# Optimization experiments

Hardware: AMD Instinct MI355X
Metric: run time of the kernel (lower is better)

Reference implementation:

```python
import jax, jax.numpy as jnp
import numpy as np

N = 100000      # nodes
E = 1600000     # edges (avg degree 16)
DIN = 512
DOUT = 64
NEG_SLOPE = 0.2


def spmm(rows, cols, vals, x, n):
    # sparse [n,n] (COO) @ dense [n,d]: out[r] += vals[e] * x[cols[e]]
    return jax.ops.segment_sum(vals[:, None] * x[cols], rows, num_segments=n)


def setup_inputs() -> dict:
    key = jax.random.key(0)
    k1, k2, k3, k4, k5 = jax.random.split(key, 5)
    features = jax.random.normal(k1, (N, DIN), dtype=jnp.float32)
    edge_rows = jax.random.randint(k2, (E,), 0, N, dtype=jnp.int32)
    edge_cols = jax.random.randint(k3, (E,), 0, N, dtype=jnp.int32)
    edge_vals = jax.random.uniform(k4, (E,), dtype=jnp.float32)
    limit = float(np.sqrt(6.0 / (DIN + DOUT)))  # xavier_uniform
    weight = jax.random.uniform(k5, (DIN, DOUT), dtype=jnp.float32,
                                minval=-limit, maxval=limit)
    return {"features": features, "weight": weight,
            "edge_rows": edge_rows, "edge_cols": edge_cols,
            "edge_vals": edge_vals}


def reference(features, weight, edge_rows, edge_cols, edge_vals):
    # active=True path: fused dense mm + LeakyReLU(0.2)
    support = jax.nn.leaky_relu(features @ weight, negative_slope=NEG_SLOPE)
    output = spmm(edge_rows, edge_cols, edge_vals, support, N)  # adj @ support
    az = spmm(edge_rows, edge_cols, edge_vals, output, N)       # adj @ output
    return (output, az)
```

## Files before the change

kernel.cpp:

```cpp
#include <hip/hip_runtime.h>
#include <hip/hip_bf16.h>

#define DIN 512
#define DOUT 64

typedef float float4v __attribute__((ext_vector_type(4)));
typedef float f32x4 __attribute__((ext_vector_type(4)));
typedef _Float16 f16x8 __attribute__((ext_vector_type(8)));
typedef unsigned int uint4v __attribute__((ext_vector_type(4)));

static __device__ __forceinline__ unsigned int pk_f16(float a, float b) {
  return __builtin_bit_cast(unsigned int, __builtin_amdgcn_cvt_pkrtz(a, b));
}

__global__ __launch_bounds__(256) void gemm_mfma_kernel(
    const float* __restrict__ X, const float* __restrict__ W,
    float* __restrict__ sup, int N)
{
  __shared__ unsigned int wlds[128][68];

  const int t    = threadIdx.x;
  const int wv   = t >> 6;
  const int lane = t & 63;
  const int l15  = lane & 15;
  const int g    = lane >> 4;

  const int rb   = blockIdx.x * 64 + wv * 16;
  const int rA   = rb + l15;
  const int rowA = rA < N ? rA : N - 1;
  const float* __restrict__ xrow = X + (size_t)rowA * DIN;

  f32x4 acc[4];
#pragma unroll
  for (int f = 0; f < 4; ++f) acc[f] = (f32x4)0.0f;

#pragma unroll 1
  for (int kh = 0; kh < 2; ++kh) {
    const int kbase = kh * 256;
    __syncthreads();
#pragma unroll
    for (int i = 0; i < 32; ++i) {
      const int idx = t + i * 256;
      const int c = idx & 63;
      const int p = idx >> 6;
      const float w0 = W[(size_t)(kbase + 2 * p) * DOUT + c];
      const float w1 = W[(size_t)(kbase + 2 * p + 1) * DOUT + c];
      wlds[p][c] = pk_f16(w0, w1);
    }
    __syncthreads();

#pragma unroll
    for (int s = 0; s < 8; ++s) {
      const int k0 = kbase + s * 32;
      const f32x4 a0 = *reinterpret_cast<const f32x4*>(xrow + k0 + g * 8);
      const f32x4 a1 = *reinterpret_cast<const f32x4*>(xrow + k0 + g * 8 + 4);
      uint4v au;
      au[0] = pk_f16(a0[0], a0[1]);
      au[1] = pk_f16(a0[2], a0[3]);
      au[2] = pk_f16(a1[0], a1[1]);
      au[3] = pk_f16(a1[2], a1[3]);
      const f16x8 afrag = __builtin_bit_cast(f16x8, au);

      const int pb = s * 16 + g * 4;
#pragma unroll
      for (int f = 0; f < 4; ++f) {
        const int c = f * 16 + l15;
        uint4v bu;
        bu[0] = wlds[pb + 0][c];
        bu[1] = wlds[pb + 1][c];
        bu[2] = wlds[pb + 2][c];
        bu[3] = wlds[pb + 3][c];
        const f16x8 bfrag = __builtin_bit_cast(f16x8, bu);
        acc[f] = __builtin_amdgcn_mfma_f32_16x16x32_f16(afrag, bfrag, acc[f], 0, 0, 0);
      }
    }
  }

  const int r0 = rb + g * 4;
#pragma unroll
  for (int f = 0; f < 4; ++f) {
    const int c = f * 16 + l15;
#pragma unroll
    for (int reg = 0; reg < 4; ++reg) {
      const int r = r0 + reg;
      if (r < N) {
        const float v = acc[f][reg];
        sup[(size_t)r * DOUT + c] = v > 0.0f ? v : 0.2f * v;
      }
    }
  }
}

__global__ __launch_bounds__(256) void hist_kernel(
    const int* __restrict__ er, int* __restrict__ cnt, int E)
{
  int i = blockIdx.x * blockDim.x + threadIdx.x;
  const int stride = gridDim.x * blockDim.x;
  for (; i < E; i += stride) atomicAdd(&cnt[er[i]], 1);
}

__global__ __launch_bounds__(256) void scan_block_kernel(
    const int* __restrict__ in, int* __restrict__ out,
    int* __restrict__ bsum, int n)
{
  __shared__ int s[256];
  const int t = threadIdx.x;
  const int gid = blockIdx.x * 256 + t;
  const int v = gid < n ? in[gid] : 0;
  s[t] = v;
  __syncthreads();
#pragma unroll
  for (int off = 1; off < 256; off <<= 1) {
    const int add = t >= off ? s[t - off] : 0;
    __syncthreads();
    s[t] += add;
    __syncthreads();
  }
  if (gid < n) out[gid] = s[t] - v;
  if (t == 255) bsum[blockIdx.x] = s[255];
}

__global__ __launch_bounds__(256) void scan_bsums_kernel(int* __restrict__ bsum, int nb)
{
  __shared__ int s[256];
  __shared__ int carry_s;
  const int t = threadIdx.x;
  if (t == 0) carry_s = 0;
  __syncthreads();
  for (int base = 0; base < nb; base += 256) {
    const int i = base + t;
    const int v = i < nb ? bsum[i] : 0;
    s[t] = v;
    __syncthreads();
#pragma unroll
    for (int off = 1; off < 256; off <<= 1) {
      const int add = t >= off ? s[t - off] : 0;
      __syncthreads();
      s[t] += add;
      __syncthreads();
    }
    const int carry = carry_s;
    if (i < nb) bsum[i] = s[t] - v + carry;
    const int total = s[255];
    __syncthreads();
    if (t == 0) carry_s = carry + total;
    __syncthreads();
  }
}

__global__ __launch_bounds__(256) void scan_add_kernel(
    int* __restrict__ out, const int* __restrict__ bsum, int n)
{
  const int gid = blockIdx.x * 256 + threadIdx.x;
  if (gid < n) out[gid] += bsum[blockIdx.x];
}

__global__ __launch_bounds__(256) void scatter_kernel(
    const int* __restrict__ er, const int* __restrict__ ec,
    const float* __restrict__ ev, int* __restrict__ cursor,
    int* __restrict__ scols, float* __restrict__ svals, int E)
{
  int i = blockIdx.x * blockDim.x + threadIdx.x;
  const int stride = gridDim.x * blockDim.x;
  for (; i < E; i += stride) {
    const int r = er[i];
    const int pos = atomicAdd(&cursor[r], 1);
    scols[pos] = ec[i];
    svals[pos] = ev[i];
  }
}

__global__ __launch_bounds__(256) void spmm_csr_kernel(
    const int* __restrict__ rowptr, const int* __restrict__ scols,
    const float* __restrict__ svals, const float* __restrict__ x,
    float* __restrict__ out, int N)
{
  const int lane = threadIdx.x & 63;
  const int row  = blockIdx.x * 4 + (threadIdx.x >> 6);
  if (row >= N) return;

  const int s = rowptr[row];
  const int e = rowptr[row + 1];
  float acc = 0.0f;

  int i = s;
  for (; i + 4 <= e; i += 4) {
    const int b = __builtin_amdgcn_readfirstlane(i);
    const int c0 = scols[b],     c1 = scols[b + 1];
    const int c2 = scols[b + 2], c3 = scols[b + 3];
    const float v0 = svals[b],     v1 = svals[b + 1];
    const float v2 = svals[b + 2], v3 = svals[b + 3];
    const float x0 = x[(size_t)c0 * DOUT + lane];
    const float x1 = x[(size_t)c1 * DOUT + lane];
    const float x2 = x[(size_t)c2 * DOUT + lane];
    const float x3 = x[(size_t)c3 * DOUT + lane];
    acc = fmaf(v0, x0, acc);
    acc = fmaf(v1, x1, acc);
    acc = fmaf(v2, x2, acc);
    acc = fmaf(v3, x3, acc);
  }
  for (; i < e; ++i) {
    const int b = __builtin_amdgcn_readfirstlane(i);
    acc = fmaf(svals[b], x[(size_t)scols[b] * DOUT + lane], acc);
  }

  out[(size_t)row * DOUT + lane] = acc;
}

extern "C" void kernel_launch(void* const* d_in, const int* in_sizes, int n_in,
                              void* d_out, int out_size, void* d_ws, size_t ws_size,
                              hipStream_t stream)
{
  const float* X  = (const float*)d_in[0];
  const float* W  = (const float*)d_in[1];
  const int*   er = (const int*)d_in[2];
  const int*   ec = (const int*)d_in[3];
  const float* ev = (const float*)d_in[4];

  const int N = in_sizes[0] / DIN;
  const int E = in_sizes[2];
  const size_t half = (size_t)N * DOUT;

  char* w = (char*)d_ws;
  float* sup    = (float*)w;                 w += half * sizeof(float);
  int*   rowptr = (int*)w;                   w += (size_t)(N + 1) * sizeof(int);
  int*   cursor = (int*)w;                   w += (size_t)(N + 1) * sizeof(int);
  int*   bsum   = (int*)w;                   w += 1024 * sizeof(int);
  int*   scols  = (int*)w;                   w += (size_t)E * sizeof(int);
  float* svals  = (float*)w;

  float* out0 = (float*)d_out;
  float* out1 = out0 + half;

  const int n_scan = N + 1;
  const int nb = (n_scan + 255) / 256;

  (void)hipMemsetAsync(cursor, 0, (size_t)n_scan * sizeof(int), stream);
  hist_kernel<<<2048, 256, 0, stream>>>(er, cursor, E);
  scan_block_kernel<<<nb, 256, 0, stream>>>(cursor, rowptr, bsum, n_scan);
  scan_bsums_kernel<<<1, 256, 0, stream>>>(bsum, nb);
  scan_add_kernel<<<nb, 256, 0, stream>>>(rowptr, bsum, n_scan);
  (void)hipMemcpyAsync(cursor, rowptr, (size_t)n_scan * sizeof(int),
                       hipMemcpyDeviceToDevice, stream);
  scatter_kernel<<<2048, 256, 0, stream>>>(er, ec, ev, cursor, scols, svals, E);

  gemm_mfma_kernel<<<(N + 63) / 64, 256, 0, stream>>>(X, W, sup, N);

  spmm_csr_kernel<<<(N + 3) / 4, 256, 0, stream>>>(rowptr, scols, svals, sup, out0, N);
  spmm_csr_kernel<<<(N + 3) / 4, 256, 0, stream>>>(rowptr, scols, svals, out0, out1, N);
}
```

Measured before the change: 388.0 us.

## Prepack fp16 weights, prefetch A rows, vector LDS loads, unroll SpMM by 8

A new small kernel converts the weight matrix once into packed fp16 pairs in column-major order. The GEMM can then fill LDS with 128-bit copies and read B fragments with one vector LDS load instead of four scalar ones. The GEMM now issues all A-row loads for a K-half before the LDS barrier so global latency overlaps the weight staging, at the cost of more registers. The SpMM gains an 8-wide unrolled gather loop to keep more memory loads in flight, and the change adds one extra kernel launch.

```diff
diff --git a/kernel.cpp b/kernel.cpp
--- a/kernel.cpp
+++ b/kernel.cpp
@@ -4,7 +4,6 @@
 #define DIN 512
 #define DOUT 64
 
-typedef float float4v __attribute__((ext_vector_type(4)));
 typedef float f32x4 __attribute__((ext_vector_type(4)));
 typedef _Float16 f16x8 __attribute__((ext_vector_type(8)));
 typedef unsigned int uint4v __attribute__((ext_vector_type(4)));
@@ -13,11 +12,21 @@
   return __builtin_bit_cast(unsigned int, __builtin_amdgcn_cvt_pkrtz(a, b));
 }
 
+__global__ __launch_bounds__(256) void pack_w_kernel(
+    const float* __restrict__ W, unsigned int* __restrict__ pw)
+{
+  const int idx = blockIdx.x * 256 + threadIdx.x;
+  const int c = idx >> 8;
+  const int p = idx & 255;
+  pw[idx] = pk_f16(W[(size_t)(2 * p) * DOUT + c],
+                   W[(size_t)(2 * p + 1) * DOUT + c]);
+}
+
 __global__ __launch_bounds__(256) void gemm_mfma_kernel(
-    const float* __restrict__ X, const float* __restrict__ W,
+    const float* __restrict__ X, const unsigned int* __restrict__ pw,
     float* __restrict__ sup, int N)
 {
-  __shared__ unsigned int wlds[128][68];
+  __shared__ unsigned int wlds[64][132];
 
   const int t    = threadIdx.x;
   const int wv   = t >> 6;
@@ -30,6 +39,9 @@
   const int rowA = rA < N ? rA : N - 1;
   const float* __restrict__ xrow = X + (size_t)rowA * DIN;
 
+  const int sc = t >> 2;
+  const int sq = t & 3;
+
   f32x4 acc[4];
 #pragma unroll
   for (int f = 0; f < 4; ++f) acc[f] = (f32x4)0.0f;
@@ -37,39 +49,38 @@
 #pragma unroll 1
   for (int kh = 0; kh < 2; ++kh) {
     const int kbase = kh * 256;
-    __syncthreads();
-#pragma unroll
-    for (int i = 0; i < 32; ++i) {
-      const int idx = t + i * 256;
-      const int c = idx & 63;
-      const int p = idx >> 6;
-      const float w0 = W[(size_t)(kbase + 2 * p) * DOUT + c];
-      const float w1 = W[(size_t)(kbase + 2 * p + 1) * DOUT + c];
-      wlds[p][c] = pk_f16(w0, w1);
-    }
-    __syncthreads();
-
+
+    f32x4 a[16];
 #pragma unroll
     for (int s = 0; s < 8; ++s) {
-      const int k0 = kbase + s * 32;
-      const f32x4 a0 = *reinterpret_cast<const f32x4*>(xrow + k0 + g * 8);
-      const f32x4 a1 = *reinterpret_cast<const f32x4*>(xrow + k0 + g * 8 + 4);
+      a[2 * s]     = *reinterpret_cast<const f32x4*>(xrow + kbase + s * 32 + g * 8);
+      a[2 * s + 1] = *reinterpret_cast<const f32x4*>(xrow + kbase + s * 32 + g * 8 + 4);
+    }
+
+    __syncthreads();
+    {
+      const unsigned int* __restrict__ src = pw + sc * 256 + kh * 128 + sq * 32;
+      uint4v* __restrict__ dst = reinterpret_cast<uint4v*>(&wlds[sc][sq * 32]);
+#pragma unroll
+      for (int i = 0; i < 8; ++i)
+        dst[i] = *(reinterpret_cast<const uint4v*>(src) + i);
+    }
+    __syncthreads();
+
+#pragma unroll
+    for (int s = 0; s < 8; ++s) {
       uint4v au;
-      au[0] = pk_f16(a0[0], a0[1]);
-      au[1] = pk_f16(a0[2], a0[3]);
-      au[2] = pk_f16(a1[0], a1[1]);
-      au[3] = pk_f16(a1[2], a1[3]);
+      au[0] = pk_f16(a[2 * s][0], a[2 * s][1]);
+      au[1] = pk_f16(a[2 * s][2], a[2 * s][3]);
+      au[2] = pk_f16(a[2 * s + 1][0], a[2 * s + 1][1]);
+      au[3] = pk_f16(a[2 * s + 1][2], a[2 * s + 1][3]);
       const f16x8 afrag = __builtin_bit_cast(f16x8, au);
 
       const int pb = s * 16 + g * 4;
 #pragma unroll
       for (int f = 0; f < 4; ++f) {
         const int c = f * 16 + l15;
-        uint4v bu;
-        bu[0] = wlds[pb + 0][c];
-        bu[1] = wlds[pb + 1][c];
-        bu[2] = wlds[pb + 2][c];
-        bu[3] = wlds[pb + 3][c];
+        const uint4v bu = *reinterpret_cast<const uint4v*>(&wlds[c][pb]);
         const f16x8 bfrag = __builtin_bit_cast(f16x8, bu);
         acc[f] = __builtin_amdgcn_mfma_f32_16x16x32_f16(afrag, bfrag, acc[f], 0, 0, 0);
       }
@@ -184,6 +195,20 @@
   float acc = 0.0f;
 
   int i = s;
+  for (; i + 8 <= e; i += 8) {
+    const int b = __builtin_amdgcn_readfirstlane(i);
+    int   cc[8];
+    float vv[8];
+    float xx[8];
+#pragma unroll
+    for (int j = 0; j < 8; ++j) cc[j] = scols[b + j];
+#pragma unroll
+    for (int j = 0; j < 8; ++j) vv[j] = svals[b + j];
+#pragma unroll
+    for (int j = 0; j < 8; ++j) xx[j] = x[(size_t)cc[j] * DOUT + lane];
+#pragma unroll
+    for (int j = 0; j < 8; ++j) acc = fmaf(vv[j], xx[j], acc);
+  }
   for (; i + 4 <= e; i += 4) {
     const int b = __builtin_amdgcn_readfirstlane(i);
     const int c0 = scols[b],     c1 = scols[b + 1];
@@ -227,7 +252,8 @@
   int*   cursor = (int*)w;                   w += (size_t)(N + 1) * sizeof(int);
   int*   bsum   = (int*)w;                   w += 1024 * sizeof(int);
   int*   scols  = (int*)w;                   w += (size_t)E * sizeof(int);
-  float* svals  = (float*)w;
+  float* svals  = (float*)w;                 w += (size_t)E * sizeof(float);
+  unsigned int* pw = (unsigned int*)w;
 
   float* out0 = (float*)d_out;
   float* out1 = out0 + half;
@@ -244,7 +270,8 @@
                        hipMemcpyDeviceToDevice, stream);
   scatter_kernel<<<2048, 256, 0, stream>>>(er, ec, ev, cursor, scols, svals, E);
 
-  gemm_mfma_kernel<<<(N + 63) / 64, 256, 0, stream>>>(X, W, sup, N);
+  pack_w_kernel<<<64, 256, 0, stream>>>(W, pw);
+  gemm_mfma_kernel<<<(N + 63) / 64, 256, 0, stream>>>(X, pw, sup, N);
 
   spmm_csr_kernel<<<(N + 3) / 4, 256, 0, stream>>>(rowptr, scols, svals, sup, out0, N);
   spmm_csr_kernel<<<(N + 3) / 4, 256, 0, stream>>>(rowptr, scols, svals, out0, out1, N);
```

New measurement: 363.5 us (median of 2 runs). 1.07x faster.
